# Kernel tuning notes

Hardware: AMD Instinct MI355X
Metric: run time of the kernel (lower is better)

Reference implementation:

```python
import jax, jax.numpy as jnp
import numpy as np

N = 100_000      # nodes
F_IN = 128       # in_channels
C = 128          # out_channels
H = 2 * C        # conv1 output dim
E = 1_000_000    # edges per graph
EPS = 1e-12      # F.normalize eps


def setup_inputs() -> dict:
    key = jax.random.key(0)
    k = jax.random.split(key, 5)
    x = jax.random.normal(k[0], (N, F_IN), jnp.float32)
    edge_index_top = jax.random.randint(k[1], (2, E), 0, N, dtype=jnp.int64)
    edge_index_last = jax.random.randint(k[2], (2, E), 0, N, dtype=jnp.int64)
    W1 = jax.random.normal(k[3], (F_IN, H), jnp.float32) / np.sqrt(F_IN)
    b1 = jnp.zeros((H,), jnp.float32)
    return {"x": x, "edge_index_top": edge_index_top,
            "edge_index_last": edge_index_last, "W1": W1, "b1": b1}


def gcn_conv(x, W, b, src, dst, n):
    """PyG GCNConv: out = D^{-1/2} (A + I) D^{-1/2} X W + b, deg over A+I."""
    xw = x @ W                                           # [N, H]
    ones = jnp.ones(src.shape[0], xw.dtype)
    deg = jax.ops.segment_sum(ones, dst, num_segments=n) + 1.0  # +1 self loop
    dinv = jax.lax.rsqrt(deg)                            # [N]
    norm = dinv[src] * dinv[dst]                         # [E]
    agg = jax.ops.segment_sum(norm[:, None] * xw[src], dst, num_segments=n)
    agg = agg + (dinv * dinv)[:, None] * xw              # self-loop term
    return agg + b


def reference(x, edge_index_top, edge_index_last, W1, b1):
    n = x.shape[0]
    # F.normalize(x, dim=1)
    xn = x / jnp.clip(jnp.linalg.norm(x, axis=1, keepdims=True), EPS)
    src_t, dst_t = edge_index_top[0], edge_index_top[1]
    ztop = gcn_conv(xn, W1, b1, src_t, dst_t, n)         # [N, H]
    # aedge = sigmoid(ztop @ ztop.T)[src, dst] without materializing NxN
    aedge = jax.nn.sigmoid(jnp.sum(ztop[src_t] * ztop[dst_t], axis=-1))  # [E]
    zlast = gcn_conv(xn, W1, b1, edge_index_last[0], edge_index_last[1], n)
    return (ztop, zlast, aedge)
```

## Files before the change

### kernel.cpp

```cpp
#include <hip/hip_runtime.h>
#include <hip/hip_bf16.h>

typedef __bf16 bf16_t;
typedef __bf16 bf16x4 __attribute__((ext_vector_type(4)));
typedef __bf16 bf16x8 __attribute__((ext_vector_type(8)));
typedef float  f32x4  __attribute__((ext_vector_type(4)));

#define N_NODES 100000
#define F_INC   128
#define HDIM    256
#define NEDGE   1000000
#define ELL_CAP 48
#define GATHER_BLKS (N_NODES / 4)
#define AEDGE_BLKS  (NEDGE / 16)
#define GEMM_BLKS   ((N_NODES / 16 + 3) / 4)
#define FILL_BLKS   ((NEDGE + 255) / 256)

__global__ void zero_cnt(int* __restrict__ cnt, int n) {
    int i = blockIdx.x * 256 + threadIdx.x;
    if (i < n) cnt[i] = 0;
}

__global__ void detect_kernel(const int* __restrict__ eit, const int* __restrict__ eil,
                              int* __restrict__ flags) {
    int lane = threadIdx.x & 63;
    const int* p = (threadIdx.x < 64) ? eit : eil;
    int s = (p[2 * lane + 1] != 0) ? 1 : 0;
    #pragma unroll
    for (int off = 1; off < 64; off <<= 1) s += __shfl_xor(s, off, 64);
    if (lane == 0) flags[(threadIdx.x < 64) ? 0 : 1] = (s == 0) ? 1 : 0;
}

__global__ void wprep_kernel(const float* __restrict__ W1, bf16_t* __restrict__ wlay,
                             bf16_t* __restrict__ xw) {
    int t = blockIdx.x * 256 + threadIdx.x;
    if (blockIdx.x == 0) {
        xw[(size_t)N_NODES * HDIM + threadIdx.x] = (bf16_t)0.f;
    }
    int j = t & 7, lane = (t >> 3) & 63, kk = (t >> 9) & 3, nt = t >> 11;
    int m = lane & 15, q = lane >> 4;
    int k = kk * 32 + q * 8 + j;
    int n = nt * 16 + m;
    wlay[t] = (bf16_t)W1[k * HDIM + n];
}

__device__ __forceinline__ void gemm_body(int w, int lane, const float* __restrict__ x,
                                          const bf16_t* __restrict__ wlay,
                                          bf16_t* __restrict__ xw) {
    if (w >= N_NODES / 16) return;
    int m = lane & 15, q = lane >> 4;
    int r0 = w * 16;
    int row = r0 + m;
    const float4* xr = (const float4*)(x + (size_t)row * F_INC);
    float4 u[8];
    #pragma unroll
    for (int kk = 0; kk < 4; kk++) {
        u[2 * kk]     = xr[kk * 8 + q * 2];
        u[2 * kk + 1] = xr[kk * 8 + q * 2 + 1];
    }
    float ss = 0.f;
    #pragma unroll
    for (int j = 0; j < 8; j++)
        ss += u[j].x * u[j].x + u[j].y * u[j].y + u[j].z * u[j].z + u[j].w * u[j].w;
    ss += __shfl_xor(ss, 16, 64);
    ss += __shfl_xor(ss, 32, 64);
    float rv = 1.0f / fmaxf(sqrtf(ss), 1e-12f);
    bf16x8 a[4];
    #pragma unroll
    for (int kk = 0; kk < 4; kk++) {
        float4 p0 = u[2 * kk], p1 = u[2 * kk + 1];
        a[kk][0] = (bf16_t)(p0.x * rv); a[kk][1] = (bf16_t)(p0.y * rv);
        a[kk][2] = (bf16_t)(p0.z * rv); a[kk][3] = (bf16_t)(p0.w * rv);
        a[kk][4] = (bf16_t)(p1.x * rv); a[kk][5] = (bf16_t)(p1.y * rv);
        a[kk][6] = (bf16_t)(p1.z * rv); a[kk][7] = (bf16_t)(p1.w * rv);
    }
    const bf16x8* wl = (const bf16x8*)wlay;
    #pragma unroll
    for (int nt = 0; nt < 16; nt++) {
        f32x4 c = {0.f, 0.f, 0.f, 0.f};
        c = __builtin_amdgcn_mfma_f32_16x16x32_bf16(a[0], wl[(nt * 4 + 0) * 64 + lane], c, 0, 0, 0);
        c = __builtin_amdgcn_mfma_f32_16x16x32_bf16(a[1], wl[(nt * 4 + 1) * 64 + lane], c, 0, 0, 0);
        c = __builtin_amdgcn_mfma_f32_16x16x32_bf16(a[2], wl[(nt * 4 + 2) * 64 + lane], c, 0, 0, 0);
        c = __builtin_amdgcn_mfma_f32_16x16x32_bf16(a[3], wl[(nt * 4 + 3) * 64 + lane], c, 0, 0, 0);
        #pragma unroll
        for (int i = 0; i < 4; i++) {
            xw[(size_t)(r0 + q * 4 + i) * HDIM + nt * 16 + m] = (bf16_t)c[i];
        }
    }
}

__device__ __forceinline__ void fill_body(int e, const int* __restrict__ ei,
                                          const int* __restrict__ flag,
                                          int* __restrict__ cnt, int* __restrict__ ell) {
    if (e >= NEDGE) return;
    int f = *flag;
    int src = ei[e << f];
    int dst = ei[(NEDGE + e) << f];
    int slot = atomicAdd(&cnt[dst], 1);
    if (slot < ELL_CAP) ell[dst * ELL_CAP + slot] = src;
}

__global__ void fill_ell(const int* __restrict__ ei, const int* __restrict__ flag,
                         int* __restrict__ cnt, int* __restrict__ ell) {
    fill_body(blockIdx.x * 256 + threadIdx.x, ei, flag, cnt, ell);
}

__global__ __launch_bounds__(256) void gemm_fill_kernel(const float* __restrict__ x,
                                                        const bf16_t* __restrict__ wlay,
                                                        bf16_t* __restrict__ xw,
                                                        const int* __restrict__ ei,
                                                        const int* __restrict__ flag,
                                                        int* __restrict__ cnt,
                                                        int* __restrict__ ell) {
    if (blockIdx.x < GEMM_BLKS) {
        gemm_body(blockIdx.x * 4 + (threadIdx.x >> 6), threadIdx.x & 63, x, wlay, xw);
    } else {
        fill_body((blockIdx.x - GEMM_BLKS) * 256 + threadIdx.x, ei, flag, cnt, ell);
    }
}

__global__ void dinvpad_kernel(const int* __restrict__ cnt, float* __restrict__ dinv,
                               int* __restrict__ ell) {
    int i = blockIdx.x * 256 + threadIdx.x;
    if (i >= N_NODES) {
        if (i == N_NODES) dinv[N_NODES] = 0.f;
        return;
    }
    int c = cnt[i];
    dinv[i] = rsqrtf((float)c + 1.0f);
    int deg = (c > ELL_CAP) ? ELL_CAP : c;
    int r4 = (deg + 3) & ~3;
    for (int s = deg; s < r4; s++) ell[i * ELL_CAP + s] = N_NODES;
}

__device__ __forceinline__ void gather_body(int i, int lane, const int* __restrict__ ell,
                                            const int* __restrict__ cnt,
                                            const float* __restrict__ dinv,
                                            const bf16_t* __restrict__ xw,
                                            const float* __restrict__ b1,
                                            float* __restrict__ out,
                                            bf16_t* __restrict__ zb) {
    float di = dinv[i];
    const bf16x4* xws = (const bf16x4*)xw;
    bf16x4 sv = xws[(size_t)i * 64 + lane];
    float acc0 = di * (float)sv.x;
    float acc1 = di * (float)sv.y;
    float acc2 = di * (float)sv.z;
    float acc3 = di * (float)sv.w;
    int deg = cnt[i];
    if (deg > ELL_CAP) deg = ELL_CAP;
    int nit = (deg + 3) >> 2;
    const int4* el4 = (const int4*)(ell + i * ELL_CAP);
    for (int b = 0; b < nit; b++) {
        int4 s = el4[b];
        float d0 = dinv[s.x], d1 = dinv[s.y], d2 = dinv[s.z], d3 = dinv[s.w];
        bf16x4 v0 = xws[(size_t)s.x * 64 + lane];
        bf16x4 v1 = xws[(size_t)s.y * 64 + lane];
        bf16x4 v2 = xws[(size_t)s.z * 64 + lane];
        bf16x4 v3 = xws[(size_t)s.w * 64 + lane];
        acc0 += d0 * (float)v0.x + d1 * (float)v1.x + d2 * (float)v2.x + d3 * (float)v3.x;
        acc1 += d0 * (float)v0.y + d1 * (float)v1.y + d2 * (float)v2.y + d3 * (float)v3.y;
        acc2 += d0 * (float)v0.z + d1 * (float)v1.z + d2 * (float)v2.z + d3 * (float)v3.z;
        acc3 += d0 * (float)v0.w + d1 * (float)v1.w + d2 * (float)v2.w + d3 * (float)v3.w;
    }
    float4 bv = ((const float4*)b1)[lane];
    float4 o;
    o.x = di * acc0 + bv.x;
    o.y = di * acc1 + bv.y;
    o.z = di * acc2 + bv.z;
    o.w = di * acc3 + bv.w;
    ((float4*)out)[(size_t)i * 64 + lane] = o;
    if (zb) {
        bf16x4 zo;
        zo.x = (bf16_t)o.x; zo.y = (bf16_t)o.y; zo.z = (bf16_t)o.z; zo.w = (bf16_t)o.w;
        ((bf16x4*)zb)[(size_t)i * 64 + lane] = zo;
    }
}

__global__ __launch_bounds__(256) void gather_top_kernel(const int* __restrict__ ell,
                                                         const int* __restrict__ cnt,
                                                         const float* __restrict__ dinv,
                                                         const bf16_t* __restrict__ xw,
                                                         const float* __restrict__ b1,
                                                         float* __restrict__ out,
                                                         bf16_t* __restrict__ zb) {
    gather_body(blockIdx.x * 4 + (threadIdx.x >> 6), threadIdx.x & 63,
                ell, cnt, dinv, xw, b1, out, zb);
}

__device__ __forceinline__ void aedge_body(int wid, int lane, const int* __restrict__ ei,
                                           const int* __restrict__ flag,
                                           const bf16_t* __restrict__ zb,
                                           float* __restrict__ aedge) {
    int sub = lane & 15;
    int e = wid * 4 + (lane >> 4);
    int f = *flag;
    int src = ei[e << f];
    int dst = ei[(NEDGE + e) << f];
    const bf16x8* z8 = (const bf16x8*)zb;
    bf16x8 a0 = z8[(size_t)src * 32 + sub * 2];
    bf16x8 a1 = z8[(size_t)src * 32 + sub * 2 + 1];
    bf16x8 b0 = z8[(size_t)dst * 32 + sub * 2];
    bf16x8 b1 = z8[(size_t)dst * 32 + sub * 2 + 1];
    float p = 0.f;
    #pragma unroll
    for (int j = 0; j < 8; j++)
        p += (float)a0[j] * (float)b0[j] + (float)a1[j] * (float)b1[j];
    #pragma unroll
    for (int off = 1; off < 16; off <<= 1) p += __shfl_xor(p, off, 64);
    if (sub == 0) aedge[e] = 1.0f / (1.0f + __expf(-p));
}

__global__ __launch_bounds__(256) void fused_last_kernel(const int* __restrict__ ell,
                                                         const int* __restrict__ cnt,
                                                         const float* __restrict__ dinv,
                                                         const bf16_t* __restrict__ xw,
                                                         const float* __restrict__ b1,
                                                         float* __restrict__ out1,
                                                         const int* __restrict__ ei_top,
                                                         const int* __restrict__ flags,
                                                         const bf16_t* __restrict__ zb,
                                                         float* __restrict__ aedge) {
    int lane = threadIdx.x & 63;
    if (blockIdx.x < GATHER_BLKS) {
        gather_body(blockIdx.x * 4 + (threadIdx.x >> 6), lane,
                    ell, cnt, dinv, xw, b1, out1, (bf16_t*)0);
    } else {
        aedge_body((blockIdx.x - GATHER_BLKS) * 4 + (threadIdx.x >> 6), lane,
                   ei_top, flags, zb, aedge);
    }
}

extern "C" void kernel_launch(void* const* d_in, const int* in_sizes, int n_in,
                              void* d_out, int out_size, void* d_ws, size_t ws_size,
                              hipStream_t stream) {
    const float* x       = (const float*)d_in[0];
    const int*   ei_top  = (const int*)d_in[1];
    const int*   ei_last = (const int*)d_in[2];
    const float* W1      = (const float*)d_in[3];
    const float* b1      = (const float*)d_in[4];
    float* out = (float*)d_out;

    char* ws = (char*)d_ws;
    bf16_t* xw     = (bf16_t*)(ws);
    bf16_t* zb     = (bf16_t*)(ws + 51201024);
    int*    ellA   = (int*)  (ws + 102401024);
    float*  dinv_t = (float*)(ws + 121601024);
    float*  dinv_l = (float*)(ws + 122001088);
    int*    cnt_t  = (int*)  (ws + 122401152);
    int*    cnt_l  = (int*)  (ws + 122801152);
    bf16_t* wlay   = (bf16_t*)(ws + 123201152);
    int*    flags  = (int*)  (ws + 123266688);

    zero_cnt<<<(2 * N_NODES + 255) / 256, 256, 0, stream>>>(cnt_t, 2 * N_NODES);
    detect_kernel<<<1, 128, 0, stream>>>(ei_top, ei_last, flags);
    wprep_kernel<<<128, 256, 0, stream>>>(W1, wlay, xw);
    gemm_fill_kernel<<<GEMM_BLKS + FILL_BLKS, 256, 0, stream>>>(x, wlay, xw,
                                                                ei_top, flags, cnt_t, ellA);
    dinvpad_kernel<<<(N_NODES + 256) / 256 + 1, 256, 0, stream>>>(cnt_t, dinv_t, ellA);
    gather_top_kernel<<<GATHER_BLKS, 256, 0, stream>>>(ellA, cnt_t, dinv_t, xw, b1, out, zb);
    fill_ell<<<FILL_BLKS, 256, 0, stream>>>(ei_last, flags + 1, cnt_l, ellA);
    dinvpad_kernel<<<(N_NODES + 256) / 256 + 1, 256, 0, stream>>>(cnt_l, dinv_l, ellA);
    fused_last_kernel<<<GATHER_BLKS + AEDGE_BLKS, 256, 0, stream>>>(
        ellA, cnt_l, dinv_l, xw, b1, out + (size_t)N_NODES * HDIM,
        ei_top, flags, zb, out + (size_t)2 * N_NODES * HDIM);
}
```

Before: 677.0 us.

## Compute edge scores per destination node using paired ELL and fuse last-graph fill

```diff
diff --git a/kernel.cpp b/kernel.cpp
--- a/kernel.cpp
+++ b/kernel.cpp
@@ -12,7 +12,6 @@
 #define NEDGE   1000000
 #define ELL_CAP 48
 #define GATHER_BLKS (N_NODES / 4)
-#define AEDGE_BLKS  (NEDGE / 16)
 #define GEMM_BLKS   ((N_NODES / 16 + 3) / 4)
 #define FILL_BLKS   ((NEDGE + 255) / 256)
 
@@ -32,10 +31,11 @@
 }
 
 __global__ void wprep_kernel(const float* __restrict__ W1, bf16_t* __restrict__ wlay,
-                             bf16_t* __restrict__ xw) {
+                             bf16_t* __restrict__ xw, bf16_t* __restrict__ zb) {
     int t = blockIdx.x * 256 + threadIdx.x;
     if (blockIdx.x == 0) {
         xw[(size_t)N_NODES * HDIM + threadIdx.x] = (bf16_t)0.f;
+        zb[(size_t)N_NODES * HDIM + threadIdx.x] = (bf16_t)0.f;
     }
     int j = t & 7, lane = (t >> 3) & 63, kk = (t >> 9) & 3, nt = t >> 11;
     int m = lane & 15, q = lane >> 4;
@@ -89,6 +89,20 @@
     }
 }
 
+__device__ __forceinline__ void fill2_body(int e, const int* __restrict__ ei,
+                                           const int* __restrict__ flag,
+                                           int* __restrict__ cnt, int* __restrict__ ell2) {
+    if (e >= NEDGE) return;
+    int f = *flag;
+    int src = ei[e << f];
+    int dst = ei[(NEDGE + e) << f];
+    int slot = atomicAdd(&cnt[dst], 1);
+    if (slot < ELL_CAP) {
+        int2 pr; pr.x = src; pr.y = e;
+        ((int2*)ell2)[(size_t)dst * ELL_CAP + slot] = pr;
+    }
+}
+
 __device__ __forceinline__ void fill_body(int e, const int* __restrict__ ei,
                                           const int* __restrict__ flag,
                                           int* __restrict__ cnt, int* __restrict__ ell) {
@@ -100,27 +114,22 @@
     if (slot < ELL_CAP) ell[dst * ELL_CAP + slot] = src;
 }
 
-__global__ void fill_ell(const int* __restrict__ ei, const int* __restrict__ flag,
-                         int* __restrict__ cnt, int* __restrict__ ell) {
-    fill_body(blockIdx.x * 256 + threadIdx.x, ei, flag, cnt, ell);
-}
-
 __global__ __launch_bounds__(256) void gemm_fill_kernel(const float* __restrict__ x,
                                                         const bf16_t* __restrict__ wlay,
                                                         bf16_t* __restrict__ xw,
                                                         const int* __restrict__ ei,
                                                         const int* __restrict__ flag,
                                                         int* __restrict__ cnt,
-                                                        int* __restrict__ ell) {
+                                                        int* __restrict__ ell2) {
     if (blockIdx.x < GEMM_BLKS) {
         gemm_body(blockIdx.x * 4 + (threadIdx.x >> 6), threadIdx.x & 63, x, wlay, xw);
     } else {
-        fill_body((blockIdx.x - GEMM_BLKS) * 256 + threadIdx.x, ei, flag, cnt, ell);
+        fill2_body((blockIdx.x - GEMM_BLKS) * 256 + threadIdx.x, ei, flag, cnt, ell2);
     }
 }
 
 __global__ void dinvpad_kernel(const int* __restrict__ cnt, float* __restrict__ dinv,
-                               int* __restrict__ ell) {
+                               int* __restrict__ ell, int paired) {
     int i = blockIdx.x * 256 + threadIdx.x;
     if (i >= N_NODES) {
         if (i == N_NODES) dinv[N_NODES] = 0.f;
@@ -130,9 +139,15 @@
     dinv[i] = rsqrtf((float)c + 1.0f);
     int deg = (c > ELL_CAP) ? ELL_CAP : c;
     int r4 = (deg + 3) & ~3;
-    for (int s = deg; s < r4; s++) ell[i * ELL_CAP + s] = N_NODES;
-}
-
+    if (paired) {
+        int2 pr; pr.x = N_NODES; pr.y = -1;
+        for (int s = deg; s < r4; s++) ((int2*)ell)[(size_t)i * ELL_CAP + s] = pr;
+    } else {
+        for (int s = deg; s < r4; s++) ell[i * ELL_CAP + s] = N_NODES;
+    }
+}
+
+template<bool PAIRED>
 __device__ __forceinline__ void gather_body(int i, int lane, const int* __restrict__ ell,
                                             const int* __restrict__ cnt,
                                             const float* __restrict__ dinv,
@@ -150,84 +165,125 @@
     int deg = cnt[i];
     if (deg > ELL_CAP) deg = ELL_CAP;
     int nit = (deg + 3) >> 2;
-    const int4* el4 = (const int4*)(ell + i * ELL_CAP);
-    for (int b = 0; b < nit; b++) {
-        int4 s = el4[b];
-        float d0 = dinv[s.x], d1 = dinv[s.y], d2 = dinv[s.z], d3 = dinv[s.w];
-        bf16x4 v0 = xws[(size_t)s.x * 64 + lane];
-        bf16x4 v1 = xws[(size_t)s.y * 64 + lane];
-        bf16x4 v2 = xws[(size_t)s.z * 64 + lane];
-        bf16x4 v3 = xws[(size_t)s.w * 64 + lane];
-        acc0 += d0 * (float)v0.x + d1 * (float)v1.x + d2 * (float)v2.x + d3 * (float)v3.x;
-        acc1 += d0 * (float)v0.y + d1 * (float)v1.y + d2 * (float)v2.y + d3 * (float)v3.y;
-        acc2 += d0 * (float)v0.z + d1 * (float)v1.z + d2 * (float)v2.z + d3 * (float)v3.z;
-        acc3 += d0 * (float)v0.w + d1 * (float)v1.w + d2 * (float)v2.w + d3 * (float)v3.w;
+    int4 sa, sb;
+    if (PAIRED) {
+        const int4* e8 = (const int4*)ell + (size_t)i * (ELL_CAP / 2);
+        sa = e8[0]; sb = e8[1];
+        for (int b = 0; b < nit; b++) {
+            int bn = (b + 1 < nit) ? (b + 1) : b;
+            int4 na = e8[2 * bn], nb = e8[2 * bn + 1];
+            int s0 = sa.x, s1 = sa.z, s2 = sb.x, s3 = sb.z;
+            float d0 = dinv[s0], d1 = dinv[s1], d2 = dinv[s2], d3 = dinv[s3];
+            bf16x4 v0 = xws[(size_t)s0 * 64 + lane];
+            bf16x4 v1 = xws[(size_t)s1 * 64 + lane];
+            bf16x4 v2 = xws[(size_t)s2 * 64 + lane];
+            bf16x4 v3 = xws[(size_t)s3 * 64 + lane];
+            acc0 += d0 * (float)v0.x + d1 * (float)v1.x + d2 * (float)v2.x + d3 * (float)v3.x;
+            acc1 += d0 * (float)v0.y + d1 * (float)v1.y + d2 * (float)v2.y + d3 * (float)v3.y;
+            acc2 += d0 * (float)v0.z + d1 * (float)v1.z + d2 * (float)v2.z + d3 * (float)v3.z;
+            acc3 += d0 * (float)v0.w + d1 * (float)v1.w + d2 * (float)v2.w + d3 * (float)v3.w;
+            sa = na; sb = nb;
+        }
+    } else {
+        const int4* el4 = (const int4*)(ell + (size_t)i * ELL_CAP);
+        sa = el4[0];
+        for (int b = 0; b < nit; b++) {
+            int bn = (b + 1 < nit) ? (b + 1) : b;
+            int4 na = el4[bn];
+            int s0 = sa.x, s1 = sa.y, s2 = sa.z, s3 = sa.w;
+            float d0 = dinv[s0], d1 = dinv[s1], d2 = dinv[s2], d3 = dinv[s3];
+            bf16x4 v0 = xws[(size_t)s0 * 64 + lane];
+            bf16x4 v1 = xws[(size_t)s1 * 64 + lane];
+            bf16x4 v2 = xws[(size_t)s2 * 64 + lane];
+            bf16x4 v3 = xws[(size_t)s3 * 64 + lane];
+            acc0 += d0 * (float)v0.x + d1 * (float)v1.x + d2 * (float)v2.x + d3 * (float)v3.x;
+            acc1 += d0 * (float)v0.y + d1 * (float)v1.y + d2 * (float)v2.y + d3 * (float)v3.y;
+            acc2 += d0 * (float)v0.z + d1 * (float)v1.z + d2 * (float)v2.z + d3 * (float)v3.z;
+            acc3 += d0 * (float)v0.w + d1 * (float)v1.w + d2 * (float)v2.w + d3 * (float)v3.w;
+            sa = na;
+        }
     }
     float4 bv = ((const float4*)b1)[lane];
-    float4 o;
-    o.x = di * acc0 + bv.x;
-    o.y = di * acc1 + bv.y;
-    o.z = di * acc2 + bv.z;
-    o.w = di * acc3 + bv.w;
-    ((float4*)out)[(size_t)i * 64 + lane] = o;
+    f32x4 o;
+    o[0] = di * acc0 + bv.x;
+    o[1] = di * acc1 + bv.y;
+    o[2] = di * acc2 + bv.z;
+    o[3] = di * acc3 + bv.w;
+    __builtin_nontemporal_store(o, (f32x4*)out + (size_t)i * 64 + lane);
     if (zb) {
         bf16x4 zo;
-        zo.x = (bf16_t)o.x; zo.y = (bf16_t)o.y; zo.z = (bf16_t)o.z; zo.w = (bf16_t)o.w;
+        zo.x = (bf16_t)o[0]; zo.y = (bf16_t)o[1]; zo.z = (bf16_t)o[2]; zo.w = (bf16_t)o[3];
         ((bf16x4*)zb)[(size_t)i * 64 + lane] = zo;
     }
 }
 
-__global__ __launch_bounds__(256) void gather_top_kernel(const int* __restrict__ ell,
-                                                         const int* __restrict__ cnt,
-                                                         const float* __restrict__ dinv,
-                                                         const bf16_t* __restrict__ xw,
-                                                         const float* __restrict__ b1,
-                                                         float* __restrict__ out,
-                                                         bf16_t* __restrict__ zb) {
-    gather_body(blockIdx.x * 4 + (threadIdx.x >> 6), threadIdx.x & 63,
-                ell, cnt, dinv, xw, b1, out, zb);
-}
-
-__device__ __forceinline__ void aedge_body(int wid, int lane, const int* __restrict__ ei,
-                                           const int* __restrict__ flag,
-                                           const bf16_t* __restrict__ zb,
-                                           float* __restrict__ aedge) {
-    int sub = lane & 15;
-    int e = wid * 4 + (lane >> 4);
-    int f = *flag;
-    int src = ei[e << f];
-    int dst = ei[(NEDGE + e) << f];
+__global__ __launch_bounds__(256) void gather_fill_kernel(const int* __restrict__ ell2,
+                                                          const int* __restrict__ cnt,
+                                                          const float* __restrict__ dinv,
+                                                          const bf16_t* __restrict__ xw,
+                                                          const float* __restrict__ b1,
+                                                          float* __restrict__ out,
+                                                          bf16_t* __restrict__ zb,
+                                                          const int* __restrict__ ei_l,
+                                                          const int* __restrict__ flag_l,
+                                                          int* __restrict__ cnt_l,
+                                                          int* __restrict__ ell_l) {
+    if (blockIdx.x < FILL_BLKS) {
+        fill_body(blockIdx.x * 256 + threadIdx.x, ei_l, flag_l, cnt_l, ell_l);
+    } else {
+        gather_body<true>((blockIdx.x - FILL_BLKS) * 4 + (threadIdx.x >> 6), threadIdx.x & 63,
+                          ell2, cnt, dinv, xw, b1, out, zb);
+    }
+}
+
+__device__ __forceinline__ void aedge_dst_body(int i, int lane, const int* __restrict__ ell2,
+                                               const int* __restrict__ cnt,
+                                               const bf16_t* __restrict__ zb,
+                                               float* __restrict__ aedge) {
+    int sub = lane & 15, g = lane >> 4;
     const bf16x8* z8 = (const bf16x8*)zb;
-    bf16x8 a0 = z8[(size_t)src * 32 + sub * 2];
-    bf16x8 a1 = z8[(size_t)src * 32 + sub * 2 + 1];
-    bf16x8 b0 = z8[(size_t)dst * 32 + sub * 2];
-    bf16x8 b1 = z8[(size_t)dst * 32 + sub * 2 + 1];
-    float p = 0.f;
-    #pragma unroll
-    for (int j = 0; j < 8; j++)
-        p += (float)a0[j] * (float)b0[j] + (float)a1[j] * (float)b1[j];
-    #pragma unroll
-    for (int off = 1; off < 16; off <<= 1) p += __shfl_xor(p, off, 64);
-    if (sub == 0) aedge[e] = 1.0f / (1.0f + __expf(-p));
-}
-
-__global__ __launch_bounds__(256) void fused_last_kernel(const int* __restrict__ ell,
-                                                         const int* __restrict__ cnt,
-                                                         const float* __restrict__ dinv,
+    bf16x8 d0 = z8[(size_t)i * 32 + sub * 2];
+    bf16x8 d1 = z8[(size_t)i * 32 + sub * 2 + 1];
+    int deg = cnt[i];
+    if (deg > ELL_CAP) deg = ELL_CAP;
+    int nit = (deg + 3) >> 2;
+    if (nit == 0) return;
+    const int2* pr = (const int2*)ell2 + (size_t)i * ELL_CAP;
+    int2 pe = pr[g];
+    for (int b = 0; b < nit; b++) {
+        int bn = (b + 1 < nit) ? (b + 1) : b;
+        int2 pn = pr[bn * 4 + g];
+        int src = pe.x, eid = pe.y;
+        bf16x8 a0 = z8[(size_t)src * 32 + sub * 2];
+        bf16x8 a1 = z8[(size_t)src * 32 + sub * 2 + 1];
+        float p = 0.f;
+        #pragma unroll
+        for (int j = 0; j < 8; j++)
+            p += (float)a0[j] * (float)d0[j] + (float)a1[j] * (float)d1[j];
+        #pragma unroll
+        for (int off = 1; off < 16; off <<= 1) p += __shfl_xor(p, off, 64);
+        if (sub == 0 && eid >= 0)
+            __builtin_nontemporal_store(1.0f / (1.0f + __expf(-p)), &aedge[eid]);
+        pe = pn;
+    }
+}
+
+__global__ __launch_bounds__(256) void fused_last_kernel(const int* __restrict__ ell_l,
+                                                         const int* __restrict__ cnt_l,
+                                                         const float* __restrict__ dinv_l,
                                                          const bf16_t* __restrict__ xw,
                                                          const float* __restrict__ b1,
                                                          float* __restrict__ out1,
-                                                         const int* __restrict__ ei_top,
-                                                         const int* __restrict__ flags,
+                                                         const int* __restrict__ ell2_t,
+                                                         const int* __restrict__ cnt_t,
                                                          const bf16_t* __restrict__ zb,
                                                          float* __restrict__ aedge) {
     int lane = threadIdx.x & 63;
-    if (blockIdx.x < GATHER_BLKS) {
-        gather_body(blockIdx.x * 4 + (threadIdx.x >> 6), lane,
-                    ell, cnt, dinv, xw, b1, out1, (bf16_t*)0);
-    } else {
-        aedge_body((blockIdx.x - GATHER_BLKS) * 4 + (threadIdx.x >> 6), lane,
-                   ei_top, flags, zb, aedge);
+    int node = (blockIdx.x >> 1) * 4 + (threadIdx.x >> 6);
+    if (blockIdx.x & 1) {
+        aedge_dst_body(node, lane, ell2_t, cnt_t, zb, aedge);
+    } else {
+        gather_body<false>(node, lane, ell_l, cnt_l, dinv_l, xw, b1, out1, (bf16_t*)0);
     }
 }
 
@@ -244,24 +300,25 @@
     char* ws = (char*)d_ws;
     bf16_t* xw     = (bf16_t*)(ws);
     bf16_t* zb     = (bf16_t*)(ws + 51201024);
-    int*    ellA   = (int*)  (ws + 102401024);
-    float*  dinv_t = (float*)(ws + 121601024);
-    float*  dinv_l = (float*)(ws + 122001088);
-    int*    cnt_t  = (int*)  (ws + 122401152);
-    int*    cnt_l  = (int*)  (ws + 122801152);
-    bf16_t* wlay   = (bf16_t*)(ws + 123201152);
-    int*    flags  = (int*)  (ws + 123266688);
+    int*    ell2t  = (int*)  (ws + 102402048);
+    int*    ell_l  = (int*)  (ws + 140802048);
+    float*  dinv_t = (float*)(ws + 160002048);
+    float*  dinv_l = (float*)(ws + 160402112);
+    int*    cnt_t  = (int*)  (ws + 160802176);
+    int*    cnt_l  = (int*)  (ws + 161202176);
+    bf16_t* wlay   = (bf16_t*)(ws + 161602176);
+    int*    flags  = (int*)  (ws + 161667712);
 
     zero_cnt<<<(2 * N_NODES + 255) / 256, 256, 0, stream>>>(cnt_t, 2 * N_NODES);
     detect_kernel<<<1, 128, 0, stream>>>(ei_top, ei_last, flags);
-    wprep_kernel<<<128, 256, 0, stream>>>(W1, wlay, xw);
+    wprep_kernel<<<128, 256, 0, stream>>>(W1, wlay, xw, zb);
     gemm_fill_kernel<<<GEMM_BLKS + FILL_BLKS, 256, 0, stream>>>(x, wlay, xw,
-                                                                ei_top, flags, cnt_t, ellA);
-    dinvpad_kernel<<<(N_NODES + 256) / 256 + 1, 256, 0, stream>>>(cnt_t, dinv_t, ellA);
-    gather_top_kernel<<<GATHER_BLKS, 256, 0, stream>>>(ellA, cnt_t, dinv_t, xw, b1, out, zb);
-    fill_ell<<<FILL_BLKS, 256, 0, stream>>>(ei_last, flags + 1, cnt_l, ellA);
-    dinvpad_kernel<<<(N_NODES + 256) / 256 + 1, 256, 0, stream>>>(cnt_l, dinv_l, ellA);
-    fused_last_kernel<<<GATHER_BLKS + AEDGE_BLKS, 256, 0, stream>>>(
-        ellA, cnt_l, dinv_l, xw, b1, out + (size_t)N_NODES * HDIM,
-        ei_top, flags, zb, out + (size_t)2 * N_NODES * HDIM);
-}
+                                                                ei_top, flags, cnt_t, ell2t);
+    dinvpad_kernel<<<(N_NODES + 256) / 256 + 1, 256, 0, stream>>>(cnt_t, dinv_t, ell2t, 1);
+    gather_fill_kernel<<<FILL_BLKS + GATHER_BLKS, 256, 0, stream>>>(
+        ell2t, cnt_t, dinv_t, xw, b1, out, zb, ei_last, flags + 1, cnt_l, ell_l);
+    dinvpad_kernel<<<(N_NODES + 256) / 256 + 1, 256, 0, stream>>>(cnt_l, dinv_l, ell_l, 0);
+    fused_last_kernel<<<2 * GATHER_BLKS, 256, 0, stream>>>(
+        ell_l, cnt_l, dinv_l, xw, b1, out + (size_t)N_NODES * HDIM,
+        ell2t, cnt_t, zb, out + (size_t)2 * N_NODES * HDIM);
+}
```

Measured after the change: 637.9 us. -5.8%, faster.
